# Kernel optimization log

Measured on AMD Instinct MI355X. Metric: run time of the kernel, lower is better.

Reference implementation:

```python
import jax, jax.numpy as jnp
import numpy as np
from jax import lax

B, U, W, E, H, Hh, C = 16, 64, 32, 300, 512, 512, 7
D = 2 * H  # bidirectional LSTM feature size


def setup_inputs() -> dict:
    key = jax.random.key(0)
    ks = jax.random.split(key, 24)
    rn = lambda k, s, sc=0.05: jax.random.normal(k, s, jnp.float32) * sc
    z = lambda n: jnp.zeros((n,), jnp.float32)
    return {
        "x": jax.random.normal(ks[0], (B, U, W, E), jnp.float32),
        # BiLSTM (PyTorch gate order i,f,g,o)
        "lstm_Wih_f": rn(ks[1], (4 * H, E)), "lstm_Whh_f": rn(ks[2], (4 * H, H)),
        "lstm_bih_f": z(4 * H), "lstm_bhh_f": z(4 * H),
        "lstm_Wih_b": rn(ks[3], (4 * H, E)), "lstm_Whh_b": rn(ks[4], (4 * H, H)),
        "lstm_bih_b": z(4 * H), "lstm_bhh_b": z(4 * H),
        # global_state_gru (GRUCell, gate order r,z,n)
        "gg_Wih": rn(ks[5], (3 * D, D)), "gg_Whh": rn(ks[6], (3 * D, D)),
        "gg_bih": z(3 * D), "gg_bhh": z(3 * D),
        # attention weight
        "Wg": rn(ks[7], (D, D)),
        # party_state_gru
        "pg_Wih": rn(ks[8], (3 * D, D)), "pg_Whh": rn(ks[9], (3 * D, D)),
        "pg_bih": z(3 * D), "pg_bhh": z(3 * D),
        # emotion_state_gru
        "eg_Wih": rn(ks[10], (3 * Hh, D)), "eg_Whh": rn(ks[11], (3 * Hh, Hh)),
        "eg_bih": z(3 * Hh), "eg_bhh": z(3 * Hh),
        # classifier
        "cls_W": rn(ks[12], (C, Hh)), "cls_b": z(C),
    }


def _gru_cell(x, h, Wih, Whh, bih, bhh):
    gi = x @ Wih.T + bih
    gh = h @ Whh.T + bhh
    ir, iz, inn = jnp.split(gi, 3, axis=-1)
    hr, hz, hn = jnp.split(gh, 3, axis=-1)
    r = jax.nn.sigmoid(ir + hr)
    zg = jax.nn.sigmoid(iz + hz)
    n = jnp.tanh(inn + r * hn)
    return (1.0 - zg) * n + zg * h


def _lstm(xs, Wih, Whh, bih, bhh, reverse):
    # xs: [W, N, E]; returns hidden states [W, N, H] in scan order
    if reverse:
        xs = xs[::-1]
    N = xs.shape[1]
    def step(carry, xt):
        h, c = carry
        g = xt @ Wih.T + bih + h @ Whh.T + bhh
        i, f, gg, o = jnp.split(g, 4, axis=-1)
        c = jax.nn.sigmoid(f) * c + jax.nn.sigmoid(i) * jnp.tanh(gg)
        h = jax.nn.sigmoid(o) * jnp.tanh(c)
        return (h, c), h
    init = (jnp.zeros((N, H), xs.dtype), jnp.zeros((N, H), xs.dtype))
    _, hs = lax.scan(step, init, xs)
    return hs


def reference(x, lstm_Wih_f, lstm_Whh_f, lstm_bih_f, lstm_bhh_f,
              lstm_Wih_b, lstm_Whh_b, lstm_bih_b, lstm_bhh_b,
              gg_Wih, gg_Whh, gg_bih, gg_bhh, Wg,
              pg_Wih, pg_Whh, pg_bih, pg_bhh,
              eg_Wih, eg_Whh, eg_bih, eg_bhh, cls_W, cls_b):
    # --- extract_features: BiLSTM over words, fwd last step + bwd first step ---
    N = B * U
    xs = jnp.swapaxes(x.reshape(N, W, E), 0, 1)  # [W, N, E]
    hf = _lstm(xs, lstm_Wih_f, lstm_Whh_f, lstm_bih_f, lstm_bhh_f, False)[-1]  # fwd @ t=W-1
    hb = _lstm(xs, lstm_Wih_b, lstm_Whh_b, lstm_bih_b, lstm_bhh_b, True)[-1]   # bwd @ t=0
    feat = jnp.concatenate([hf, hb], axis=-1).reshape(B, U, D)

    # --- detect_emotions: sequential GRU recurrence with growing-history attention ---
    utt = jnp.swapaxes(feat, 0, 1)  # [U, B, D]
    tpos = jnp.arange(U + 1)

    def step(carry, sx):
        hist, p0, p1, e = carry  # hist: [U+1, B, D], hist[0] = zeros
        u, i = sx
        is0 = (i % 2) == 0
        p = jnp.where(is0, p0, p1)
        g_new = _gru_cell(u + p, hist[i], gg_Wih, gg_Whh, gg_bih, gg_bhh)
        hist = hist.at[i + 1].set(g_new)
        # attention over history states 0..i (excludes just-appended g_new)
        q = u @ Wg                                  # [B, D]
        scores = jnp.einsum('bd,tbd->tb', q, hist)  # [U+1, B]
        scores = jnp.where((tpos <= i)[:, None], scores, -1e9)
        w = jax.nn.softmax(scores, axis=0)
        ctx = jnp.einsum('tb,tbd->bd', w, hist)
        p_new = _gru_cell(u + ctx, p, pg_Wih, pg_Whh, pg_bih, pg_bhh)
        p0 = jnp.where(is0, p_new, p0)
        p1 = jnp.where(is0, p1, p_new)
        e = _gru_cell(p_new, e, eg_Wih, eg_Whh, eg_bih, eg_bhh)
        return (hist, p0, p1, e), e

    init = (jnp.zeros((U + 1, B, D), feat.dtype),
            jnp.zeros((B, D), feat.dtype),
            jnp.zeros((B, D), feat.dtype),
            jnp.zeros((B, Hh), feat.dtype))
    _, es = lax.scan(step, init, (utt, jnp.arange(U)))  # es: [U, B, Hh]

    out = jnp.swapaxes(es, 0, 1) @ cls_W.T + cls_b  # [B, U, C]
    return out
```

## Files before the change

kernel.cpp:

```cpp
#include <hip/hip_runtime.h>
#include <hip/hip_bf16.h>


#define DEV static __device__ __forceinline__

typedef __attribute__((ext_vector_type(4))) float f32x4;
typedef __attribute__((ext_vector_type(8))) short bf16x8;
typedef __attribute__((ext_vector_type(8))) unsigned short u16x8;

DEV float sigmoidf_(float x) { return 1.0f / (1.0f + __expf(-x)); }

DEV unsigned short f2bf(float f) {
    union { float f; unsigned u; } v; v.f = f;
    unsigned r = v.u + 0x7FFFu + ((v.u >> 16) & 1u);
    return (unsigned short)(r >> 16);
}

DEV bf16x8 cvt8(f32x4 a, f32x4 b) {
    bf16x8 r;
    r[0] = (short)f2bf(a[0]); r[1] = (short)f2bf(a[1]);
    r[2] = (short)f2bf(a[2]); r[3] = (short)f2bf(a[3]);
    r[4] = (short)f2bf(b[0]); r[5] = (short)f2bf(b[1]);
    r[6] = (short)f2bf(b[2]); r[7] = (short)f2bf(b[3]);
    return r;
}


__global__ __launch_bounds__(256) void k_build_xpad(const float* __restrict__ x,
                                                    unsigned short* __restrict__ xpad) {
    int g = blockIdx.x * 256 + threadIdx.x;
    if (g >= 2621440) return;
    int kg = (g % 40) * 8;
    int n = (g / 40) & 1023;
    int t = (g / (40 * 1024)) & 31;
    int dir = g / (40 * 1024 * 32);
    int teff = dir ? (31 - t) : t;
    const float* xr = x + ((size_t)n * 32 + teff) * 300;
    u16x8 o;
#pragma unroll
    for (int e = 0; e < 8; ++e) {
        int kp = kg + e;
        o[e] = (kp < 300) ? f2bf(xr[kp]) : (unsigned short)0;
    }
    *(u16x8*)&xpad[(size_t)g * 8] = o;
}

__global__ __launch_bounds__(256) void k_build_wcat(
    const float* __restrict__ wihf, const float* __restrict__ whhf,
    const float* __restrict__ wihb, const float* __restrict__ whhb,
    unsigned short* __restrict__ wcat) {
    int gt = blockIdx.x * 256 + threadIdx.x;
    if (gt >= 2 * 2048 * 832) return;
    int k = gt % 832;
    int j = (gt / 832) & 2047;
    int dir = gt / (832 * 2048);
    const float* wih = dir ? wihb : wihf;
    const float* whh = dir ? whhb : whhf;
    float v = 0.0f;
    if (k < 300) v = wih[j * 300 + k];
    else if (k >= 320) v = whh[j * 512 + (k - 320)];
    wcat[gt] = f2bf(v);
}

__global__ __launch_bounds__(256) void k_cat_w(const float* __restrict__ Wih,
                                               const float* __restrict__ Whh,
                                               unsigned short* __restrict__ out,
                                               int K1, int K2) {
    int j = blockIdx.x;
    int KW = K1 + K2;
    const float* a = Wih + (size_t)j * K1;
    const float* b = Whh + (size_t)j * K2;
    unsigned short* o = out + (size_t)j * KW;
    for (int k = threadIdx.x; k < KW; k += 256)
        o[k] = f2bf(k < K1 ? a[k] : b[k - K1]);
}

__global__ __launch_bounds__(256) void k_transpose_bf(const float* __restrict__ in,
                                                      unsigned short* __restrict__ out) {
    __shared__ float t[64][65];
    int tid = threadIdx.x;
    int r0 = blockIdx.y * 64, c0 = blockIdx.x * 64;
#pragma unroll
    for (int rep = 0; rep < 16; ++rep) {
        int lin = rep * 256 + tid;
        int r = lin >> 6, c = lin & 63;
        t[r][c] = in[(size_t)(r0 + r) * 1024 + c0 + c];
    }
    __syncthreads();
#pragma unroll
    for (int rep = 0; rep < 16; ++rep) {
        int lin = rep * 256 + tid;
        int d = lin >> 6, k = lin & 63;
        out[(size_t)(c0 + d) * 1024 + r0 + k] = f2bf(t[k][d]);
    }
}


__global__ __launch_bounds__(256) void k_lstm_step(
    const unsigned short* __restrict__ xpad,
    const unsigned short* __restrict__ hbfin,
    const unsigned short* __restrict__ wcat,
    float* __restrict__ cbuf,
    float* __restrict__ hbuf,
    unsigned short* __restrict__ hbfout,
    const float* __restrict__ bihf, const float* __restrict__ bhhf,
    const float* __restrict__ bihb, const float* __restrict__ bhhb,
    int t) {
    __shared__ unsigned short As[64][72];
    __shared__ unsigned short Ws[4][64][72];

    const int tid  = threadIdx.x;
    const int br   = blockIdx.x;
    const int bc   = blockIdx.y;
    const int row0 = br * 64;
    const int dir  = row0 >> 10;
    const int n0   = row0 & 1023;
    const int j0   = bc * 64;

    const int lane = tid & 63;
    const int wv   = tid >> 6;
    const int wm   = (wv >> 1) * 32;
    const int wn   = (wv & 1) * 32;
    const int srow = tid >> 2;
    const int sk0  = (tid & 3) * 16;
    const int arow = lane & 15;
    const int kq   = (lane >> 4) * 8;

    f32x4 acc[4][2][2];
#pragma unroll
    for (int g = 0; g < 4; ++g)
#pragma unroll
        for (int i = 0; i < 2; ++i)
#pragma unroll
            for (int j = 0; j < 2; ++j) acc[g][i][j] = (f32x4){0.f, 0.f, 0.f, 0.f};

    const unsigned short* xrow = xpad + (((size_t)dir * 32 + t) * 1024 + n0 + srow) * 320;
    const unsigned short* hrow = hbfin + ((size_t)dir * 1024 + n0 + srow) * 512;
    const unsigned short* wr0 = wcat + ((size_t)dir * 2048 + j0 + srow) * 832;

    for (int kt = 0; kt < 13; ++kt) {
        const unsigned short* asrc = (kt < 5) ? (xrow + kt * 64) : (hrow + (kt * 64 - 320));
        *(u16x8*)&As[srow][sk0]     = *(const u16x8*)&asrc[sk0];
        *(u16x8*)&As[srow][sk0 + 8] = *(const u16x8*)&asrc[sk0 + 8];
#pragma unroll
        for (int g = 0; g < 4; ++g) {
            const unsigned short* wsrc = wr0 + (size_t)g * 512 * 832 + kt * 64;
            *(u16x8*)&Ws[g][srow][sk0]     = *(const u16x8*)&wsrc[sk0];
            *(u16x8*)&Ws[g][srow][sk0 + 8] = *(const u16x8*)&wsrc[sk0 + 8];
        }
        __syncthreads();
#pragma unroll
        for (int kk = 0; kk < 64; kk += 32) {
            bf16x8 af[2];
            af[0] = *(const bf16x8*)&As[wm + arow][kk + kq];
            af[1] = *(const bf16x8*)&As[wm + 16 + arow][kk + kq];
#pragma unroll
            for (int g = 0; g < 4; ++g) {
                bf16x8 b0 = *(const bf16x8*)&Ws[g][wn + arow][kk + kq];
                bf16x8 b1 = *(const bf16x8*)&Ws[g][wn + 16 + arow][kk + kq];
                acc[g][0][0] = __builtin_amdgcn_mfma_f32_16x16x32_bf16(af[0], b0, acc[g][0][0], 0, 0, 0);
                acc[g][0][1] = __builtin_amdgcn_mfma_f32_16x16x32_bf16(af[0], b1, acc[g][0][1], 0, 0, 0);
                acc[g][1][0] = __builtin_amdgcn_mfma_f32_16x16x32_bf16(af[1], b0, acc[g][1][0], 0, 0, 0);
                acc[g][1][1] = __builtin_amdgcn_mfma_f32_16x16x32_bf16(af[1], b1, acc[g][1][1], 0, 0, 0);
            }
        }
        __syncthreads();
    }

    const float* bih = dir ? bihb : bihf;
    const float* bhh = dir ? bhhb : bhhf;
    const int rrow = (lane >> 4) * 4;
    const int ccol = lane & 15;
#pragma unroll
    for (int i = 0; i < 2; ++i)
#pragma unroll
        for (int j = 0; j < 2; ++j) {
            const int nr = n0 + wm + i * 16 + rrow;
            const int gd = j0 + wn + j * 16 + ccol;
            const float bi = bih[gd]        + bhh[gd];
            const float bf = bih[gd + 512]  + bhh[gd + 512];
            const float bg = bih[gd + 1024] + bhh[gd + 1024];
            const float bo = bih[gd + 1536] + bhh[gd + 1536];
#pragma unroll
            for (int r = 0; r < 4; ++r) {
                const float iv = acc[0][i][j][r] + bi;
                const float fv = acc[1][i][j][r] + bf;
                const float gv = acc[2][i][j][r] + bg;
                const float ov = acc[3][i][j][r] + bo;
                const size_t idx = (size_t)dir * 524288 + (size_t)(nr + r) * 512 + gd;
                const float cv = sigmoidf_(fv) * cbuf[idx] + sigmoidf_(iv) * tanhf(gv);
                const float hv = sigmoidf_(ov) * tanhf(cv);
                cbuf[idx] = cv;
                hbuf[idx] = hv;
                hbfout[idx] = f2bf(hv);
            }
        }
}

__global__ __launch_bounds__(256) void k_feat(const float* __restrict__ h,
                                              float* __restrict__ feat,
                                              unsigned short* __restrict__ featbf) {
    int idx = blockIdx.x * 256 + threadIdx.x;
    int n = idx >> 10;
    int d = idx & 1023;
    float v = (d < 512) ? h[(size_t)n * 512 + d]
                        : h[524288 + (size_t)n * 512 + (d - 512)];
    feat[idx] = v;
    featbf[idx] = f2bf(v);
}

__global__ __launch_bounds__(256) void k_gemm_bt(
    const unsigned short* __restrict__ A, int lda,
    const unsigned short* __restrict__ B, int ldb,
    float* __restrict__ C, int ldc, int K) {
    __shared__ unsigned short As[64][72];
    __shared__ unsigned short Bs[64][72];
    const int tid = threadIdx.x;
    const int m0 = blockIdx.x * 64;
    const int n0 = blockIdx.y * 64;
    const int lane = tid & 63;
    const int wvq = tid >> 6;
    const int wm = (wvq >> 1) * 32;
    const int wn = (wvq & 1) * 32;
    const int srow = tid >> 2;
    const int sk0 = (tid & 3) * 16;
    const int arow = lane & 15;
    const int kq = (lane >> 4) * 8;
    f32x4 acc[2][2];
#pragma unroll
    for (int i = 0; i < 2; ++i)
#pragma unroll
        for (int j = 0; j < 2; ++j) acc[i][j] = (f32x4){0.f, 0.f, 0.f, 0.f};
    const unsigned short* ar = A + (size_t)(m0 + srow) * lda;
    const unsigned short* br = B + (size_t)(n0 + srow) * ldb;
    for (int kb = 0; kb < K; kb += 64) {
        int k0 = kb + sk0;
        *(u16x8*)&As[srow][sk0]     = *(const u16x8*)&ar[k0];
        *(u16x8*)&As[srow][sk0 + 8] = *(const u16x8*)&ar[k0 + 8];
        *(u16x8*)&Bs[srow][sk0]     = *(const u16x8*)&br[k0];
        *(u16x8*)&Bs[srow][sk0 + 8] = *(const u16x8*)&br[k0 + 8];
        __syncthreads();
#pragma unroll
        for (int kk = 0; kk < 64; kk += 32) {
            bf16x8 af[2], bfg[2];
#pragma unroll
            for (int i = 0; i < 2; ++i) {
                af[i]  = *(const bf16x8*)&As[wm + i * 16 + arow][kk + kq];
                bfg[i] = *(const bf16x8*)&Bs[wn + i * 16 + arow][kk + kq];
            }
#pragma unroll
            for (int i = 0; i < 2; ++i)
#pragma unroll
                for (int j = 0; j < 2; ++j)
                    acc[i][j] = __builtin_amdgcn_mfma_f32_16x16x32_bf16(
                        af[i], bfg[j], acc[i][j], 0, 0, 0);
        }
        __syncthreads();
    }
    const int rrow = (lane >> 4) * 4;
    const int ccol = lane & 15;
#pragma unroll
    for (int i = 0; i < 2; ++i)
#pragma unroll
        for (int j = 0; j < 2; ++j) {
            int mr = m0 + wm + i * 16 + rrow;
            int nc = n0 + wn + j * 16 + ccol;
#pragma unroll
            for (int r = 0; r < 4; ++r)
                C[(size_t)(mr + r) * ldc + nc] = acc[i][j][r];
        }
}


DEV void gru_block16(
    int c0,
    const float* __restrict__ aBase, long aStride,
    const float* __restrict__ addBase, long addStride,
    const float* __restrict__ hBase, long hStride,
    const unsigned short* __restrict__ W,
    const float* __restrict__ bih, const float* __restrict__ bhh,
    float* __restrict__ outBase, long outStride,
    int D, int K1, int K2,
    float (*sred)[3][16][17]) {
    const int tid = threadIdx.x;
    const int lane = tid & 63;
    const int wv = tid >> 6;
    const int p = lane & 15;
    const int kq = (lane >> 4) * 8;
    const int KW = K1 + K2;
    const int Kc = KW >> 4;
    const int kStart = wv * Kc;
    const bool hasAdd = (addBase != nullptr);

    f32x4 accA[3], accB[3];
#pragma unroll
    for (int g = 0; g < 3; ++g) {
        accA[g] = (f32x4){0.f, 0.f, 0.f, 0.f};
        accB[g] = (f32x4){0.f, 0.f, 0.f, 0.f};
    }
    const unsigned short* w0 = W + (size_t)(c0 + p) * KW;
    const unsigned short* w1 = w0 + (size_t)D * KW;
    const unsigned short* w2 = w1 + (size_t)D * KW;
    const float* aRow = aBase + (size_t)p * aStride;
    const float* addRow = hasAdd ? addBase + (size_t)p * addStride : (const float*)0;
    const float* hRow = hBase + (size_t)p * hStride;

    for (int k = kStart; k < kStart + Kc; k += 32) {
        const int kk = k + kq;
        f32x4 x0, x1;
        const bool inA = (k < K1);
        if (inA) {
            x0 = *(const f32x4*)&aRow[kk];
            x1 = *(const f32x4*)&aRow[kk + 4];
            if (hasAdd) {
                f32x4 y0 = *(const f32x4*)&addRow[kk];
                f32x4 y1 = *(const f32x4*)&addRow[kk + 4];
                x0 = x0 + y0; x1 = x1 + y1;
            }
        } else {
            x0 = *(const f32x4*)&hRow[kk - K1];
            x1 = *(const f32x4*)&hRow[kk - K1 + 4];
        }
        bf16x8 af = cvt8(x0, x1);
        bf16x8 b0 = *(const bf16x8*)&w0[kk];
        bf16x8 b1 = *(const bf16x8*)&w1[kk];
        bf16x8 b2 = *(const bf16x8*)&w2[kk];
        if (inA) {
            accA[0] = __builtin_amdgcn_mfma_f32_16x16x32_bf16(af, b0, accA[0], 0, 0, 0);
            accA[1] = __builtin_amdgcn_mfma_f32_16x16x32_bf16(af, b1, accA[1], 0, 0, 0);
            accA[2] = __builtin_amdgcn_mfma_f32_16x16x32_bf16(af, b2, accA[2], 0, 0, 0);
        } else {
            accB[0] = __builtin_amdgcn_mfma_f32_16x16x32_bf16(af, b0, accB[0], 0, 0, 0);
            accB[1] = __builtin_amdgcn_mfma_f32_16x16x32_bf16(af, b1, accB[1], 0, 0, 0);
            accB[2] = __builtin_amdgcn_mfma_f32_16x16x32_bf16(af, b2, accB[2], 0, 0, 0);
        }
    }

    const int mB = (lane >> 4) * 4;
    const int m = tid >> 4;
    const int d = tid & 15;

#pragma unroll
    for (int g = 0; g < 3; ++g)
#pragma unroll
        for (int r = 0; r < 4; ++r)
            sred[wv][g][mB + r][p] = accA[g][r];
    __syncthreads();
    float ir = 0.f, iz = 0.f, inn = 0.f;
    if (tid < 256) {
#pragma unroll
        for (int w = 0; w < 16; ++w) {
            ir += sred[w][0][m][d]; iz += sred[w][1][m][d]; inn += sred[w][2][m][d];
        }
    }
    __syncthreads();
#pragma unroll
    for (int g = 0; g < 3; ++g)
#pragma unroll
        for (int r = 0; r < 4; ++r)
            sred[wv][g][mB + r][p] = accB[g][r];
    __syncthreads();
    if (tid < 256) {
        float hr = 0.f, hz = 0.f, hn = 0.f;
#pragma unroll
        for (int w = 0; w < 16; ++w) {
            hr += sred[w][0][m][d]; hz += sred[w][1][m][d]; hn += sred[w][2][m][d];
        }
        int gd = c0 + d;
        float rg = sigmoidf_(ir + bih[gd] + hr + bhh[gd]);
        float zg = sigmoidf_(iz + bih[gd + D] + hz + bhh[gd + D]);
        float ng = tanhf(inn + bih[gd + 2 * D] + rg * (hn + bhh[gd + 2 * D]));
        float hp = hBase[(size_t)m * hStride + gd];
        outBase[(size_t)m * outStride + gd] = (1.0f - zg) * ng + zg * hp;
    }
}

DEV void attn_block(int b, int i, const float* __restrict__ q_all,
                    const float* __restrict__ hist, float* __restrict__ ctxout,
                    float* __restrict__ satt) {
    const int tid = threadIdx.x;
    const int lane = tid & 63;
    const int wv = tid >> 6;
    const float* qb = q_all + ((size_t)b * 64 + i) * 1024;
    for (int t = wv; t <= i; t += 16) {
        const float* hrow = hist + ((size_t)t * 16 + b) * 1024;
        float s = 0.f;
        for (int dd = lane; dd < 1024; dd += 64) s += qb[dd] * hrow[dd];
        for (int o = 32; o > 0; o >>= 1) s += __shfl_down(s, o);
        if (lane == 0) satt[t] = s;
    }
    __syncthreads();
    if (wv == 0) {
        float v = (lane <= i) ? satt[lane] : -3.0e38f;
        float mx = v;
        for (int o = 32; o > 0; o >>= 1) mx = fmaxf(mx, __shfl_xor(mx, o));
        float e = (lane <= i) ? __expf(v - mx) : 0.f;
        float sum = e;
        for (int o = 32; o > 0; o >>= 1) sum += __shfl_xor(sum, o);
        if (lane <= i) satt[lane] = e / sum;
    }
    __syncthreads();
    const int dd = tid;
    float s = 0.f;
    for (int t = 0; t <= i; ++t)
        s += satt[t] * hist[((size_t)t * 16 + b) * 1024 + dd];
    ctxout[(size_t)b * 1024 + dd] = s;
}

__global__ __launch_bounds__(1024) void k_dec_A(
    const float* __restrict__ feat, const float* __restrict__ q_all,
    float* __restrict__ hist, const float* __restrict__ psel,
    const unsigned short* __restrict__ ggW,
    const float* __restrict__ gg_bih, const float* __restrict__ gg_bhh,
    float* __restrict__ ctxb,
    const float* __restrict__ pn_prev, const float* __restrict__ e_prev,
    float* __restrict__ es_prev_out,
    const unsigned short* __restrict__ egW,
    const float* __restrict__ eg_bih, const float* __restrict__ eg_bhh,
    int i) {
    __shared__ float sred[16][3][16][17];
    __shared__ float satt[80];
    const int blk = blockIdx.x;
    if (blk < 64) {
        if (i >= 64) return;
        gru_block16(blk * 16, feat + (size_t)i * 1024, 65536L, psel, 1024L,
                    hist + (size_t)i * 16384, 1024L, ggW, gg_bih, gg_bhh,
                    hist + (size_t)(i + 1) * 16384, 1024L, 1024, 1024, 1024, sred);
    } else if (blk < 80) {
        if (i >= 64) return;
        attn_block(blk - 64, i, q_all, hist, ctxb, satt);
    } else {
        if (i < 1) return;
        gru_block16((blk - 80) * 16, pn_prev, 1024L, (const float*)0, 0L,
                    e_prev, 512L, egW, eg_bih, eg_bhh,
                    es_prev_out, 512L, 512, 1024, 512, sred);
    }
}

__global__ __launch_bounds__(1024) void k_dec_B(
    const float* __restrict__ feat, const float* __restrict__ ctxb,
    const float* __restrict__ psel,
    const unsigned short* __restrict__ pgW,
    const float* __restrict__ pg_bih, const float* __restrict__ pg_bhh,
    float* __restrict__ pn, int i) {
    __shared__ float sred[16][3][16][17];
    gru_block16(blockIdx.x * 16, feat + (size_t)i * 1024, 65536L, ctxb, 1024L,
                psel, 1024L, pgW, pg_bih, pg_bhh, pn, 1024L, 1024, 1024, 1024, sred);
}

__global__ __launch_bounds__(256) void k_cls(const float* __restrict__ es,
                                             const float* __restrict__ W,
                                             const float* __restrict__ bias,
                                             float* __restrict__ out) {
    int blk = blockIdx.x;
    int b = blk >> 6;
    int u = blk & 63;
    const float* erow = es + ((size_t)u * 16 + b) * 512;
    int tid = threadIdx.x;
    int lane = tid & 63;
    int wv = tid >> 6;
    for (int c = wv; c < 7; c += 4) {
        float s = 0.f;
        for (int k = lane; k < 512; k += 64) s += erow[k] * W[(size_t)c * 512 + k];
        for (int o = 32; o > 0; o >>= 1) s += __shfl_down(s, o);
        if (lane == 0) out[((size_t)b * 64 + u) * 7 + c] = s + bias[c];
    }
}


extern "C" void kernel_launch(void* const* d_in, const int* in_sizes, int n_in,
                              void* d_out, int out_size, void* d_ws, size_t ws_size,
                              hipStream_t stream) {
    (void)in_sizes; (void)n_in; (void)out_size; (void)ws_size;
    const float* x          = (const float*)d_in[0];
    const float* lstm_Wih_f = (const float*)d_in[1];
    const float* lstm_Whh_f = (const float*)d_in[2];
    const float* lstm_bih_f = (const float*)d_in[3];
    const float* lstm_bhh_f = (const float*)d_in[4];
    const float* lstm_Wih_b = (const float*)d_in[5];
    const float* lstm_Whh_b = (const float*)d_in[6];
    const float* lstm_bih_b = (const float*)d_in[7];
    const float* lstm_bhh_b = (const float*)d_in[8];
    const float* gg_Wih = (const float*)d_in[9];
    const float* gg_Whh = (const float*)d_in[10];
    const float* gg_bih = (const float*)d_in[11];
    const float* gg_bhh = (const float*)d_in[12];
    const float* Wg     = (const float*)d_in[13];
    const float* pg_Wih = (const float*)d_in[14];
    const float* pg_Whh = (const float*)d_in[15];
    const float* pg_bih = (const float*)d_in[16];
    const float* pg_bhh = (const float*)d_in[17];
    const float* eg_Wih = (const float*)d_in[18];
    const float* eg_Whh = (const float*)d_in[19];
    const float* eg_bih = (const float*)d_in[20];
    const float* eg_bhh = (const float*)d_in[21];
    const float* cls_W  = (const float*)d_in[22];
    const float* cls_b  = (const float*)d_in[23];

    char* wsp = (char*)d_ws;
    size_t off = 0;
    auto alloc = [&](size_t bytes) -> void* {
        void* p = wsp + off;
        off += (bytes + 255) & ~(size_t)255;
        return p;
    };
    unsigned short* xpad = (unsigned short*)alloc((size_t)20971520 * 2);
    unsigned short* wcat = (unsigned short*)alloc((size_t)2 * 2048 * 832 * 2);
    unsigned short* hbf2 = (unsigned short*)alloc((size_t)2 * 2 * 1024 * 512 * 2);
    float* hbuf  = (float*)alloc((size_t)2 * 1024 * 512 * 4);
    float* cbuf  = (float*)alloc((size_t)2 * 1024 * 512 * 4);
    float* feat  = (float*)alloc((size_t)1024 * 1024 * 4);
    unsigned short* featbf = (unsigned short*)alloc((size_t)1024 * 1024 * 2);
    float* hist  = (float*)alloc((size_t)65 * 16 * 1024 * 4);
    float* q_all = (float*)alloc((size_t)1024 * 1024 * 4);
    float* ctxb  = (float*)alloc((size_t)16 * 1024 * 4);
    float* pnew  = (float*)alloc((size_t)64 * 16 * 1024 * 4);
    float* esb   = (float*)alloc((size_t)64 * 16 * 512 * 4);
    float* zeroD = (float*)alloc((size_t)16 * 1024 * 4);
    float* zeroH = (float*)alloc((size_t)16 * 512 * 4);
    unsigned short* WgTb = (unsigned short*)alloc((size_t)1024 * 1024 * 2);
    unsigned short* ggWb = (unsigned short*)xpad;
    unsigned short* pgWb = (unsigned short*)((char*)xpad + 12582912);
    unsigned short* egWb = (unsigned short*)((char*)xpad + 25165824);

    hipMemsetAsync(hbf2, 0, (size_t)2 * 1024 * 512 * 2, stream);
    hipMemsetAsync(cbuf, 0, (size_t)2 * 1024 * 512 * 4, stream);
    hipMemsetAsync(hist, 0, (size_t)65 * 16 * 1024 * 4, stream);
    hipMemsetAsync(zeroD, 0, (size_t)16 * 1024 * 4, stream);
    hipMemsetAsync(zeroH, 0, (size_t)16 * 512 * 4, stream);

    k_build_xpad<<<10240, 256, 0, stream>>>(x, xpad);
    k_build_wcat<<<13312, 256, 0, stream>>>(lstm_Wih_f, lstm_Whh_f, lstm_Wih_b, lstm_Whh_b, wcat);

    const size_t HP = (size_t)2 * 1024 * 512;
    for (int t = 0; t < 32; ++t) {
        k_lstm_step<<<dim3(32, 8), 256, 0, stream>>>(
            xpad, hbf2 + (t & 1) * HP, wcat, cbuf, hbuf, hbf2 + ((t + 1) & 1) * HP,
            lstm_bih_f, lstm_bhh_f, lstm_bih_b, lstm_bhh_b, t);
    }
    k_feat<<<4096, 256, 0, stream>>>(hbuf, feat, featbf);

    k_cat_w<<<3072, 256, 0, stream>>>(gg_Wih, gg_Whh, ggWb, 1024, 1024);
    k_cat_w<<<3072, 256, 0, stream>>>(pg_Wih, pg_Whh, pgWb, 1024, 1024);
    k_cat_w<<<1536, 256, 0, stream>>>(eg_Wih, eg_Whh, egWb, 1024, 512);
    k_transpose_bf<<<dim3(16, 16), 256, 0, stream>>>(Wg, WgTb);
    k_gemm_bt<<<dim3(16, 16), 256, 0, stream>>>(featbf, 1024, WgTb, 1024, q_all, 1024, 1024);

    float* p0 = zeroD;
    float* p1 = zeroD;
    for (int i = 0; i <= 64; ++i) {
        float* psel = (i & 1) ? p1 : p0;
        const float* pn_prev = (i >= 1) ? pnew + (size_t)(i - 1) * 16384 : (const float*)0;
        const float* e_prev  = (i >= 2) ? esb + (size_t)(i - 2) * 8192 : zeroH;
        float* es_prev_out   = (i >= 1) ? esb + (size_t)(i - 1) * 8192 : (float*)0;
        k_dec_A<<<112, 1024, 0, stream>>>(feat, q_all, hist, psel,
                                          ggWb, gg_bih, gg_bhh, ctxb,
                                          pn_prev, e_prev, es_prev_out,
                                          egWb, eg_bih, eg_bhh, i);
        if (i < 64) {
            float* pn = pnew + (size_t)i * 16384;
            k_dec_B<<<64, 1024, 0, stream>>>(feat, ctxb, psel, pgWb, pg_bih, pg_bhh, pn, i);
            if (i & 1) p1 = pn; else p0 = pn;
        }
    }
    k_cls<<<1024, 256, 0, stream>>>(esb, cls_W, cls_b, (float*)d_out);
}
```

Baseline: 3.120 ms.

## Fuse decoder time loop into one persistent kernel with grid barriers

Replaces the 129 per-step decoder launches (k_dec_A/k_dec_B) with a single persistent kernel of 176 blocks. The blocks sync through an atomic grid barrier and run global GRU, attention, party GRU and emotion GRU as a pipelined wavefront over 66 phases. Per-step context is stored in a full buffer that reuses hbuf, so stages for different utterances can overlap. This removes launch overhead and lets the party and attention stages overlap across steps. In exchange it depends on all 176 blocks being co-resident, since the spin barrier deadlocks otherwise, and it adds barrier latency at every phase.

```diff
diff --git a/kernel.cpp b/kernel.cpp
--- a/kernel.cpp
+++ b/kernel.cpp
@@ -3,6 +3,9 @@
 
 
 #define DEV static __device__ __forceinline__
+
+#define DEC_NBLK 176
+#define DEC_PHASES 66
 
 typedef __attribute__((ext_vector_type(4))) float f32x4;
 typedef __attribute__((ext_vector_type(8))) short bf16x8;
@@ -373,6 +376,7 @@
         float hp = hBase[(size_t)m * hStride + gd];
         outBase[(size_t)m * outStride + gd] = (1.0f - zg) * ng + zg * hp;
     }
+    __syncthreads();
 }
 
 DEV void attn_block(int b, int i, const float* __restrict__ q_all,
@@ -405,47 +409,80 @@
     for (int t = 0; t <= i; ++t)
         s += satt[t] * hist[((size_t)t * 16 + b) * 1024 + dd];
     ctxout[(size_t)b * 1024 + dd] = s;
-}
-
-__global__ __launch_bounds__(1024) void k_dec_A(
+    __syncthreads();
+}
+
+DEV void gridbar(unsigned* cnt, unsigned* gen, int ph) {
+    __syncthreads();
+    if (threadIdx.x == 0) {
+        __threadfence();
+        unsigned old = __hip_atomic_fetch_add(cnt, 1u, __ATOMIC_ACQ_REL,
+                                              __HIP_MEMORY_SCOPE_AGENT);
+        const unsigned target = (unsigned)(ph + 1) * (unsigned)DEC_NBLK;
+        if (old == target - 1u) {
+            __hip_atomic_store(gen, (unsigned)(ph + 1), __ATOMIC_RELEASE,
+                               __HIP_MEMORY_SCOPE_AGENT);
+        } else {
+            while (__hip_atomic_load(gen, __ATOMIC_ACQUIRE,
+                                     __HIP_MEMORY_SCOPE_AGENT) < (unsigned)(ph + 1))
+                __builtin_amdgcn_s_sleep(8);
+        }
+    }
+    __syncthreads();
+}
+
+__global__ __launch_bounds__(1024) void k_decoder(
     const float* __restrict__ feat, const float* __restrict__ q_all,
-    float* __restrict__ hist, const float* __restrict__ psel,
+    float* __restrict__ hist, float* __restrict__ ctx_all,
     const unsigned short* __restrict__ ggW,
     const float* __restrict__ gg_bih, const float* __restrict__ gg_bhh,
-    float* __restrict__ ctxb,
-    const float* __restrict__ pn_prev, const float* __restrict__ e_prev,
-    float* __restrict__ es_prev_out,
+    const unsigned short* __restrict__ pgW,
+    const float* __restrict__ pg_bih, const float* __restrict__ pg_bhh,
     const unsigned short* __restrict__ egW,
     const float* __restrict__ eg_bih, const float* __restrict__ eg_bhh,
-    int i) {
+    float* __restrict__ pnew, float* __restrict__ esb,
+    const float* __restrict__ zeroD, const float* __restrict__ zeroH,
+    unsigned* __restrict__ bar) {
     __shared__ float sred[16][3][16][17];
     __shared__ float satt[80];
     const int blk = blockIdx.x;
-    if (blk < 64) {
-        if (i >= 64) return;
-        gru_block16(blk * 16, feat + (size_t)i * 1024, 65536L, psel, 1024L,
-                    hist + (size_t)i * 16384, 1024L, ggW, gg_bih, gg_bhh,
-                    hist + (size_t)(i + 1) * 16384, 1024L, 1024, 1024, 1024, sred);
-    } else if (blk < 80) {
-        if (i >= 64) return;
-        attn_block(blk - 64, i, q_all, hist, ctxb, satt);
-    } else {
-        if (i < 1) return;
-        gru_block16((blk - 80) * 16, pn_prev, 1024L, (const float*)0, 0L,
-                    e_prev, 512L, egW, eg_bih, eg_bhh,
-                    es_prev_out, 512L, 512, 1024, 512, sred);
-    }
-}
-
-__global__ __launch_bounds__(1024) void k_dec_B(
-    const float* __restrict__ feat, const float* __restrict__ ctxb,
-    const float* __restrict__ psel,
-    const unsigned short* __restrict__ pgW,
-    const float* __restrict__ pg_bih, const float* __restrict__ pg_bhh,
-    float* __restrict__ pn, int i) {
-    __shared__ float sred[16][3][16][17];
-    gru_block16(blockIdx.x * 16, feat + (size_t)i * 1024, 65536L, ctxb, 1024L,
-                psel, 1024L, pgW, pg_bih, pg_bhh, pn, 1024L, 1024, 1024, 1024, sred);
+    unsigned* cnt = bar;
+    unsigned* gen = bar + 64;
+
+    for (int ph = 0; ph < DEC_PHASES; ++ph) {
+        if (blk < 64) {
+            const int i = ph;
+            if (i < 64) {
+                const float* psel = (i >= 2) ? pnew + (size_t)(i - 2) * 16384 : zeroD;
+                gru_block16(blk * 16, feat + (size_t)i * 1024, 65536L, psel, 1024L,
+                            hist + (size_t)i * 16384, 1024L, ggW, gg_bih, gg_bhh,
+                            hist + (size_t)(i + 1) * 16384, 1024L, 1024, 1024, 1024, sred);
+            }
+        } else if (blk < 128) {
+            const int i = ph - 1;
+            if (i >= 0 && i < 64) {
+                const float* psel = (i >= 2) ? pnew + (size_t)(i - 2) * 16384 : zeroD;
+                gru_block16((blk - 64) * 16, feat + (size_t)i * 1024, 65536L,
+                            ctx_all + (size_t)i * 16384, 1024L,
+                            psel, 1024L, pgW, pg_bih, pg_bhh,
+                            pnew + (size_t)i * 16384, 1024L, 1024, 1024, 1024, sred);
+            }
+        } else if (blk < 144) {
+            const int i = ph;
+            if (i < 64)
+                attn_block(blk - 128, i, q_all, hist, ctx_all + (size_t)i * 16384, satt);
+        } else {
+            const int i = ph - 2;
+            if (i >= 0 && i < 64) {
+                const float* ep = (i >= 1) ? esb + (size_t)(i - 1) * 8192 : zeroH;
+                gru_block16((blk - 144) * 16, pnew + (size_t)i * 16384, 1024L,
+                            (const float*)0, 0L,
+                            ep, 512L, egW, eg_bih, eg_bhh,
+                            esb + (size_t)i * 8192, 512L, 512, 1024, 512, sred);
+            }
+        }
+        gridbar(cnt, gen, ph);
+    }
 }
 
 __global__ __launch_bounds__(256) void k_cls(const float* __restrict__ es,
@@ -513,21 +550,23 @@
     unsigned short* featbf = (unsigned short*)alloc((size_t)1024 * 1024 * 2);
     float* hist  = (float*)alloc((size_t)65 * 16 * 1024 * 4);
     float* q_all = (float*)alloc((size_t)1024 * 1024 * 4);
-    float* ctxb  = (float*)alloc((size_t)16 * 1024 * 4);
     float* pnew  = (float*)alloc((size_t)64 * 16 * 1024 * 4);
     float* esb   = (float*)alloc((size_t)64 * 16 * 512 * 4);
     float* zeroD = (float*)alloc((size_t)16 * 1024 * 4);
     float* zeroH = (float*)alloc((size_t)16 * 512 * 4);
     unsigned short* WgTb = (unsigned short*)alloc((size_t)1024 * 1024 * 2);
+    unsigned* bar = (unsigned*)alloc(512);
     unsigned short* ggWb = (unsigned short*)xpad;
     unsigned short* pgWb = (unsigned short*)((char*)xpad + 12582912);
     unsigned short* egWb = (unsigned short*)((char*)xpad + 25165824);
+    float* ctx_all = hbuf;
 
     hipMemsetAsync(hbf2, 0, (size_t)2 * 1024 * 512 * 2, stream);
     hipMemsetAsync(cbuf, 0, (size_t)2 * 1024 * 512 * 4, stream);
     hipMemsetAsync(hist, 0, (size_t)65 * 16 * 1024 * 4, stream);
     hipMemsetAsync(zeroD, 0, (size_t)16 * 1024 * 4, stream);
     hipMemsetAsync(zeroH, 0, (size_t)16 * 512 * 4, stream);
+    hipMemsetAsync(bar, 0, 512, stream);
 
     k_build_xpad<<<10240, 256, 0, stream>>>(x, xpad);
     k_build_wcat<<<13312, 256, 0, stream>>>(lstm_Wih_f, lstm_Whh_f, lstm_Wih_b, lstm_Whh_b, wcat);
@@ -546,22 +585,12 @@
     k_transpose_bf<<<dim3(16, 16), 256, 0, stream>>>(Wg, WgTb);
     k_gemm_bt<<<dim3(16, 16), 256, 0, stream>>>(featbf, 1024, WgTb, 1024, q_all, 1024, 1024);
 
-    float* p0 = zeroD;
-    float* p1 = zeroD;
-    for (int i = 0; i <= 64; ++i) {
-        float* psel = (i & 1) ? p1 : p0;
-        const float* pn_prev = (i >= 1) ? pnew + (size_t)(i - 1) * 16384 : (const float*)0;
-        const float* e_prev  = (i >= 2) ? esb + (size_t)(i - 2) * 8192 : zeroH;
-        float* es_prev_out   = (i >= 1) ? esb + (size_t)(i - 1) * 8192 : (float*)0;
-        k_dec_A<<<112, 1024, 0, stream>>>(feat, q_all, hist, psel,
-                                          ggWb, gg_bih, gg_bhh, ctxb,
-                                          pn_prev, e_prev, es_prev_out,
-                                          egWb, eg_bih, eg_bhh, i);
-        if (i < 64) {
-            float* pn = pnew + (size_t)i * 16384;
-            k_dec_B<<<64, 1024, 0, stream>>>(feat, ctxb, psel, pgWb, pg_bih, pg_bhh, pn, i);
-            if (i & 1) p1 = pn; else p0 = pn;
-        }
-    }
+    k_decoder<<<DEC_NBLK, 1024, 0, stream>>>(
+        feat, q_all, hist, ctx_all,
+        ggWb, gg_bih, gg_bhh,
+        pgWb, pg_bih, pg_bhh,
+        egWb, eg_bih, eg_bhh,
+        pnew, esb, zeroD, zeroH, bar);
+
     k_cls<<<1024, 256, 0, stream>>>(esb, cls_W, cls_b, (float*)d_out);
 }
```

After: 5.138 ms. +64.7%, slower.
